# Kernel optimization log

Measured on AMD Instinct MI355X. Metric: run time of the kernel, lower is better.

The kernel has to match this reference:

```python
import jax, jax.numpy as jnp
import numpy as np

E = 4096          # num edges
M = 12            # sum(m_size) = 5+4+3
C = 64            # sphere_channels
D = 64            # m_output_channels
M0 = 5            # m_size[0]
XD = 64           # extra_m0_output_channels
EC = 128          # edge channel dims (edge_channels_list = [128,128,128])
MAIN = M * C * D          # 49152
EXTRA = M0 * C * XD       # 20480
TOTAL = MAIN + EXTRA      # 69632


def setup_inputs() -> dict:
    key = jax.random.key(0)
    ks = jax.random.split(key, 8)
    def xavier(k, shape):
        fan_in, fan_out = shape
        lim = jnp.sqrt(6.0 / (fan_in + fan_out))
        return jax.random.uniform(k, shape, jnp.float32, -lim, lim)
    return {
        "x": jax.random.normal(ks[0], (E, M, C), jnp.float32),
        "x_edge": jax.random.normal(ks[1], (E, EC), jnp.float32),
        "W1": xavier(ks[2], (EC, EC)),
        "b1": jnp.zeros((EC,), jnp.float32),
        "W2": xavier(ks[3], (EC, EC)),
        "b2": jnp.zeros((EC,), jnp.float32),
        "W3": xavier(ks[4], (EC, TOTAL)),
        "b3": jnp.zeros((TOTAL,), jnp.float32),
    }


def reference(x, x_edge, W1, b1, W2, b2, W3, b3):
    # edge MLP: Dense -> silu -> Dense -> silu -> Dense
    h = jax.nn.silu(x_edge @ W1 + b1)
    h = jax.nn.silu(h @ W2 + b2)
    edge_weights = h @ W3 + b3                      # (E, TOTAL) huge intermediate
    main_w = edge_weights[:, :MAIN].reshape(E, M, C, D)
    out = jnp.einsum('bmcd,bmc->bmd', main_w, x)    # (E, M, D)
    extra_w = edge_weights[:, MAIN:].reshape(E, M0, C, XD)
    x_0 = x[:, :M0, :]
    x_0_gating = jnp.einsum('bmcd,bmc->bd', extra_w, x_0)  # (E, XD)
    return out, x_0_gating
```

## Files before the change

### kernel.cpp

```cpp
#include <hip/hip_runtime.h>
#include <hip/hip_bf16.h>

#define E 4096
#define M 12
#define C 64
#define D 64
#define M0 5
#define XD 64
#define EC 128
#define MAIN (M*C*D)
#define EXTRA (M0*C*XD)
#define TOTAL (MAIN+EXTRA)
#define NSLICE 17
#define KDIM 8256

typedef float  f32x4  __attribute__((ext_vector_type(4)));
typedef __bf16 bf16x8 __attribute__((ext_vector_type(8)));
typedef unsigned int u32x4 __attribute__((ext_vector_type(4)));
typedef unsigned int u32x2 __attribute__((ext_vector_type(2)));

typedef const __attribute__((address_space(1))) void gvoid;
typedef __attribute__((address_space(3))) void lvoid;

__device__ __forceinline__ float silu_f(float v) { return v / (1.0f + __expf(-v)); }

__device__ __forceinline__ unsigned short f2bf(float f) {
    unsigned u = __builtin_bit_cast(unsigned, f);
    u += 0x7FFFu + ((u >> 16) & 1u);
    return (unsigned short)(u >> 16);
}
__device__ __forceinline__ unsigned pack2(float a, float b) {
    return (unsigned)f2bf(a) | ((unsigned)f2bf(b) << 16);
}
__device__ __forceinline__ float asf(unsigned u) { return __builtin_bit_cast(float, u); }

__global__ __launch_bounds__(256) void mlp_kernel(
    const float* __restrict__ x_edge, const float* __restrict__ W1,
    const float* __restrict__ b1, const float* __restrict__ W2,
    const float* __restrict__ b2, unsigned short* __restrict__ h2t)
{
    __shared__ float xe[16][128];
    __shared__ float h1s[16][128];
    const int t  = threadIdx.x;
    const int b0 = blockIdx.x * 16;
    const int j  = t & 127;
    const int rh = t >> 7;

    #pragma unroll
    for (int i = 0; i < 8; ++i) {
        int lin = t + i * 256;
        int r = lin >> 7, k = lin & 127;
        xe[r][k] = x_edge[(size_t)(b0 + r) * EC + k];
    }
    __syncthreads();
    {
        float acc[8];
        float bb = b1[j];
        #pragma unroll
        for (int it = 0; it < 8; ++it) acc[it] = bb;
        for (int k = 0; k < 128; ++k) {
            float w = W1[k * EC + j];
            #pragma unroll
            for (int it = 0; it < 8; ++it) acc[it] += xe[rh + it * 2][k] * w;
        }
        #pragma unroll
        for (int it = 0; it < 8; ++it) h1s[rh + it * 2][j] = silu_f(acc[it]);
    }
    __syncthreads();
    {
        float acc[8];
        float bb = b2[j];
        #pragma unroll
        for (int it = 0; it < 8; ++it) acc[it] = bb;
        for (int k = 0; k < 128; ++k) {
            float w = W2[k * EC + j];
            #pragma unroll
            for (int it = 0; it < 8; ++it) acc[it] += h1s[rh + it * 2][k] * w;
        }
        #pragma unroll
        for (int it = 0; it < 8; ++it)
            h2t[(size_t)j * E + (b0 + rh + it * 2)] = f2bf(silu_f(acc[it]));
    }
    if (t < 16) h2t[(size_t)128 * E + b0 + t] = 0x3F80;
}

__global__ __launch_bounds__(256) void w3t_kernel(
    const float* __restrict__ W3, const float* __restrict__ b3,
    unsigned short* __restrict__ w3t)
{
    const int k = blockIdx.x;
    const int s = blockIdx.y;
    __shared__ float tile[64][68];
    const int t = threadIdx.x;
    const float* src = ((k < 128) ? (W3 + (size_t)k * TOTAL) : b3) + s * 4096;

    const int c  = t >> 2;
    const int dp = (t & 3) * 16;
    #pragma unroll
    for (int i = 0; i < 4; ++i) {
        float4 v = *reinterpret_cast<const float4*>(src + c * 64 + dp + i * 4);
        *reinterpret_cast<float4*>(&tile[c][dp + i * 4]) = v;
    }
    __syncthreads();

    const int d  = t >> 2;
    const int cp = (t & 3) * 16;
    unsigned u[8];
    #pragma unroll
    for (int i = 0; i < 8; ++i)
        u[i] = pack2(tile[cp + 2 * i][d], tile[cp + 2 * i + 1][d]);
    unsigned short* dst = w3t + (size_t)(s * 64 + d) * KDIM + k * 64 + cp;
    *reinterpret_cast<u32x4*>(dst)     = u32x4{u[0], u[1], u[2], u[3]};
    *reinterpret_cast<u32x4*>(dst + 8) = u32x4{u[4], u[5], u[6], u[7]};
}

__global__ __launch_bounds__(256, 3) void gemm_kernel(
    const float* __restrict__ x, const unsigned short* __restrict__ h2t,
    const unsigned short* __restrict__ w3t,
    float* __restrict__ out, unsigned short* __restrict__ outp,
    float* __restrict__ gatep)
{
    __shared__ __align__(16) unsigned short h2s[65 * 256];
    __shared__ __align__(16) unsigned short Bs[2][4096];

    const int t  = threadIdx.x;
    const int w  = t >> 6;
    const int l  = t & 63;
    const int p  = l >> 4;
    const int lr = l & 15;

    const int bid  = blockIdx.x;
    const int slot = (bid & 7) * 92 + (bid >> 3);
    const int grp  = slot >> 4;
    const int bx   = slot & 15;
    int s, kz, k0, nk;
    if (grp < 36) { s = grp / 3; kz = grp % 3; k0 = kz * 43; nk = 43; }
    else { int gg = grp - 36; s = 12 + (gg >> 1); kz = gg & 1; k0 = kz * 65; nk = 65 - kz; }
    const int b0 = bx * 256;
    const int m  = (s < 12) ? s : (s - 12);

    {
        const char* h2g = (const char*)(h2t + (size_t)k0 * E + b0);
        const int total = nk * 512;
        for (int lin = t * 16; lin < total; lin += 4096) {
            int kl = lin >> 9, off = lin & 511;
            *reinterpret_cast<u32x4*>((char*)h2s + lin) =
                *reinterpret_cast<const u32x4*>(h2g + (size_t)kl * (E * 2) + off);
        }
    }

    u32x4 xa[4][2];
    #pragma unroll
    for (int rf = 0; rf < 4; ++rf)
        #pragma unroll
        for (int s2 = 0; s2 < 2; ++s2) {
            const float* xp = x + (size_t)(b0 + w * 64 + rf * 16 + lr) * (M * C)
                              + m * 64 + s2 * 32 + p * 8;
            float4 a = *reinterpret_cast<const float4*>(xp);
            float4 b = *reinterpret_cast<const float4*>(xp + 4);
            xa[rf][s2] = u32x4{pack2(a.x, a.y), pack2(a.z, a.w),
                               pack2(b.x, b.y), pack2(b.z, b.w)};
        }

    const unsigned short* gsrc[2];
    #pragma unroll
    for (int q = 0; q < 2; ++q)
        gsrc[q] = w3t + (size_t)(s * 64 + w * 16 + lr) * KDIM
                  + (size_t)k0 * 64 + (q * 4 + p) * 8;

#define STAGE(buf, kr)                                                          \
    {                                                                           \
        _Pragma("unroll")                                                       \
        for (int q = 0; q < 2; ++q)                                             \
            __builtin_amdgcn_global_load_lds(                                   \
                (gvoid*)(gsrc[q] + (size_t)(kr) * 64),                          \
                (lvoid*)(&Bs[buf][(w * 2 + q) * 512]), 16, 0, 0);               \
    }

    f32x4 acc[4][4];
    #pragma unroll
    for (int a = 0; a < 4; ++a)
        #pragma unroll
        for (int b = 0; b < 4; ++b) acc[a][b] = f32x4{0.f, 0.f, 0.f, 0.f};
    const f32x4 zf = {0.f, 0.f, 0.f, 0.f};

    STAGE(0, 0);
    __syncthreads();

    int cur = 0;
    for (int kr = 0; kr < nk; ++kr) {
        if (kr + 1 < nk) STAGE(cur ^ 1, kr + 1);

        float h[4][4];
        #pragma unroll
        for (int rf = 0; rf < 4; ++rf) {
            u32x2 hv = *reinterpret_cast<const u32x2*>(
                &h2s[kr * 256 + w * 64 + rf * 16 + p * 4]);
            h[rf][0] = asf(hv.x << 16);
            h[rf][1] = asf(hv.x & 0xFFFF0000u);
            h[rf][2] = asf(hv.y << 16);
            h[rf][3] = asf(hv.y & 0xFFFF0000u);
        }
        #pragma unroll
        for (int cf = 0; cf < 4; ++cf) {
            u32x4 B0 = *reinterpret_cast<const u32x4*>(&Bs[cur][(cf * 2 + 0) * 512 + l * 8]);
            u32x4 B1 = *reinterpret_cast<const u32x4*>(&Bs[cur][(cf * 2 + 1) * 512 + l * 8]);
            #pragma unroll
            for (int rf = 0; rf < 4; ++rf) {
                f32x4 tt = __builtin_amdgcn_mfma_f32_16x16x32_bf16(
                    __builtin_bit_cast(bf16x8, xa[rf][0]),
                    __builtin_bit_cast(bf16x8, B0), zf, 0, 0, 0);
                tt = __builtin_amdgcn_mfma_f32_16x16x32_bf16(
                    __builtin_bit_cast(bf16x8, xa[rf][1]),
                    __builtin_bit_cast(bf16x8, B1), tt, 0, 0, 0);
                acc[rf][cf][0] += h[rf][0] * tt[0];
                acc[rf][cf][1] += h[rf][1] * tt[1];
                acc[rf][cf][2] += h[rf][2] * tt[2];
                acc[rf][cf][3] += h[rf][3] * tt[3];
            }
        }
        __syncthreads();
        cur ^= 1;
    }
#undef STAGE

    if (s < 12) {
        if (kz == 0) {
            #pragma unroll
            for (int rf = 0; rf < 4; ++rf)
                #pragma unroll
                for (int cf = 0; cf < 4; ++cf)
                    #pragma unroll
                    for (int r = 0; r < 4; ++r) {
                        int b = b0 + w * 64 + rf * 16 + p * 4 + r;
                        int d = cf * 16 + lr;
                        out[(size_t)b * (M * D) + s * D + d] = acc[rf][cf][r];
                    }
        } else {
            unsigned short* ob = outp + (size_t)(kz - 1) * (E * M * D);
            #pragma unroll
            for (int rf = 0; rf < 4; ++rf)
                #pragma unroll
                for (int cf = 0; cf < 4; ++cf)
                    #pragma unroll
                    for (int r = 0; r < 4; ++r) {
                        int b = b0 + w * 64 + rf * 16 + p * 4 + r;
                        int d = cf * 16 + lr;
                        ob[(size_t)b * (M * D) + s * D + d] = f2bf(acc[rf][cf][r]);
                    }
        }
    } else {
        float* gp = gatep + (size_t)((s - 12) * 2 + kz) * (E * 64);
        #pragma unroll
        for (int rf = 0; rf < 4; ++rf)
            #pragma unroll
            for (int cf = 0; cf < 4; ++cf)
                #pragma unroll
                for (int r = 0; r < 4; ++r) {
                    int b = b0 + w * 64 + rf * 16 + p * 4 + r;
                    int d = cf * 16 + lr;
                    gp[(size_t)b * 64 + d] = acc[rf][cf][r];
                }
    }
}

__global__ __launch_bounds__(256) void reduce_kernel(
    float* __restrict__ out, const unsigned short* __restrict__ outp,
    const float* __restrict__ gatep)
{
    const int MAIN4 = E * M * D / 4;
    int i = blockIdx.x * 256 + threadIdx.x;
    if (i < MAIN4) {
        float4 a = reinterpret_cast<float4*>(out)[i];
        u32x2 p0 = *reinterpret_cast<const u32x2*>(outp + (size_t)i * 4);
        u32x2 p1 = *reinterpret_cast<const u32x2*>(outp + (size_t)E * M * D + (size_t)i * 4);
        a.x += asf(p0.x << 16)        + asf(p1.x << 16);
        a.y += asf(p0.x & 0xFFFF0000u) + asf(p1.x & 0xFFFF0000u);
        a.z += asf(p0.y << 16)        + asf(p1.y << 16);
        a.w += asf(p0.y & 0xFFFF0000u) + asf(p1.y & 0xFFFF0000u);
        reinterpret_cast<float4*>(out)[i] = a;
    } else {
        int j = i - MAIN4;
        const float4* g4 = reinterpret_cast<const float4*>(gatep);
        float4 sum = make_float4(0.f, 0.f, 0.f, 0.f);
        #pragma unroll
        for (int q = 0; q < 10; ++q) {
            float4 v = g4[(size_t)q * 65536 + j];
            sum.x += v.x; sum.y += v.y; sum.z += v.z; sum.w += v.w;
        }
        reinterpret_cast<float4*>(out + (size_t)E * M * D)[j] = sum;
    }
}

extern "C" void kernel_launch(void* const* d_in, const int* in_sizes, int n_in,
                              void* d_out, int out_size, void* d_ws, size_t ws_size,
                              hipStream_t stream)
{
    const float* x      = (const float*)d_in[0];
    const float* x_edge = (const float*)d_in[1];
    const float* W1     = (const float*)d_in[2];
    const float* b1     = (const float*)d_in[3];
    const float* W2     = (const float*)d_in[4];
    const float* b2     = (const float*)d_in[5];
    const float* W3     = (const float*)d_in[6];
    const float* b3     = (const float*)d_in[7];

    float* out = (float*)d_out;

    char* ws = (char*)d_ws;
    unsigned short* w3t   = (unsigned short*)ws;
    unsigned short* h2t   = (unsigned short*)(ws + 17965056);
    unsigned short* outp  = (unsigned short*)(ws + 19021824);
    float*          gatep = (float*)(ws + 31604736);

    mlp_kernel<<<E / 16, 256, 0, stream>>>(x_edge, W1, b1, W2, b2, h2t);
    w3t_kernel<<<dim3(129, NSLICE), 256, 0, stream>>>(W3, b3, w3t);
    gemm_kernel<<<736, 256, 0, stream>>>(x, h2t, w3t, out, outp, gatep);
    reduce_kernel<<<3328, 256, 0, stream>>>(out, outp, gatep);
}
```

Measured before the change: 140.9 us.

## Triple-buffer B tiles with explicit waitcnt pipeline and uniform 3-way K split

Replaces the double-buffered B staging with a three-stage ring and explicit vmcnt/lgkmcnt waits plus raw barriers, so global-to-LDS loads run further ahead of the MFMA loop. MFMA sections are bracketed with s_setprio. The extra-gating slices now use the same 3-way K split of 43 as the main slices, giving uniform blocks (816 instead of 736) and a smaller h2 LDS buffer. Gate partials are stored as bf16 across 15 partial buffers to cut write and reduce traffic, at some precision cost.

```diff
diff --git a/kernel.cpp b/kernel.cpp
--- a/kernel.cpp
+++ b/kernel.cpp
@@ -13,6 +13,7 @@
 #define TOTAL (MAIN+EXTRA)
 #define NSLICE 17
 #define KDIM 8256
+#define NKB 43
 
 typedef float  f32x4  __attribute__((ext_vector_type(4)));
 typedef __bf16 bf16x8 __attribute__((ext_vector_type(8)));
@@ -116,12 +117,11 @@
 
 __global__ __launch_bounds__(256, 3) void gemm_kernel(
     const float* __restrict__ x, const unsigned short* __restrict__ h2t,
-    const unsigned short* __restrict__ w3t,
-    float* __restrict__ out, unsigned short* __restrict__ outp,
-    float* __restrict__ gatep)
-{
-    __shared__ __align__(16) unsigned short h2s[65 * 256];
-    __shared__ __align__(16) unsigned short Bs[2][4096];
+    const unsigned short* __restrict__ w3t, float* __restrict__ out,
+    unsigned short* __restrict__ outp, unsigned short* __restrict__ gatep)
+{
+    __shared__ __align__(16) unsigned short h2s[NKB * 256];
+    __shared__ __align__(16) unsigned short Bs[3][4096];
 
     const int t  = threadIdx.x;
     const int w  = t >> 6;
@@ -130,19 +130,18 @@
     const int lr = l & 15;
 
     const int bid  = blockIdx.x;
-    const int slot = (bid & 7) * 92 + (bid >> 3);
+    const int slot = (bid & 7) * 102 + (bid >> 3);
     const int grp  = slot >> 4;
     const int bx   = slot & 15;
-    int s, kz, k0, nk;
-    if (grp < 36) { s = grp / 3; kz = grp % 3; k0 = kz * 43; nk = 43; }
-    else { int gg = grp - 36; s = 12 + (gg >> 1); kz = gg & 1; k0 = kz * 65; nk = 65 - kz; }
-    const int b0 = bx * 256;
-    const int m  = (s < 12) ? s : (s - 12);
+    const int s    = grp / 3;
+    const int kz   = grp % 3;
+    const int k0   = kz * NKB;
+    const int b0   = bx * 256;
+    const int m    = (s < 12) ? s : (s - 12);
 
     {
         const char* h2g = (const char*)(h2t + (size_t)k0 * E + b0);
-        const int total = nk * 512;
-        for (int lin = t * 16; lin < total; lin += 4096) {
+        for (int lin = t * 16; lin < NKB * 512; lin += 4096) {
             int kl = lin >> 9, off = lin & 511;
             *reinterpret_cast<u32x4*>((char*)h2s + lin) =
                 *reinterpret_cast<const u32x4*>(h2g + (size_t)kl * (E * 2) + off);
@@ -184,45 +183,72 @@
         for (int b = 0; b < 4; ++b) acc[a][b] = f32x4{0.f, 0.f, 0.f, 0.f};
     const f32x4 zf = {0.f, 0.f, 0.f, 0.f};
 
+#define KBODY(kr, curv)                                                         \
+    {                                                                           \
+        float h[4][4];                                                          \
+        _Pragma("unroll")                                                       \
+        for (int rf = 0; rf < 4; ++rf) {                                        \
+            u32x2 hv = *reinterpret_cast<const u32x2*>(                         \
+                &h2s[(kr) * 256 + w * 64 + rf * 16 + p * 4]);                   \
+            h[rf][0] = asf(hv.x << 16);                                         \
+            h[rf][1] = asf(hv.x & 0xFFFF0000u);                                 \
+            h[rf][2] = asf(hv.y << 16);                                         \
+            h[rf][3] = asf(hv.y & 0xFFFF0000u);                                 \
+        }                                                                       \
+        __builtin_amdgcn_s_setprio(1);                                          \
+        _Pragma("unroll")                                                       \
+        for (int cf = 0; cf < 4; ++cf) {                                        \
+            u32x4 B0 = *reinterpret_cast<const u32x4*>(                         \
+                &Bs[curv][(cf * 2 + 0) * 512 + l * 8]);                         \
+            u32x4 B1 = *reinterpret_cast<const u32x4*>(                         \
+                &Bs[curv][(cf * 2 + 1) * 512 + l * 8]);                         \
+            _Pragma("unroll")                                                   \
+            for (int rf = 0; rf < 4; ++rf) {                                    \
+                f32x4 tt = __builtin_amdgcn_mfma_f32_16x16x32_bf16(             \
+                    __builtin_bit_cast(bf16x8, xa[rf][0]),                      \
+                    __builtin_bit_cast(bf16x8, B0), zf, 0, 0, 0);               \
+                tt = __builtin_amdgcn_mfma_f32_16x16x32_bf16(                   \
+                    __builtin_bit_cast(bf16x8, xa[rf][1]),                      \
+                    __builtin_bit_cast(bf16x8, B1), tt, 0, 0, 0);               \
+                acc[rf][cf][0] += h[rf][0] * tt[0];                             \
+                acc[rf][cf][1] += h[rf][1] * tt[1];                             \
+                acc[rf][cf][2] += h[rf][2] * tt[2];                             \
+                acc[rf][cf][3] += h[rf][3] * tt[3];                             \
+            }                                                                   \
+        }                                                                       \
+        __builtin_amdgcn_s_setprio(0);                                          \
+    }
+
+    __syncthreads();
+
     STAGE(0, 0);
-    __syncthreads();
+    STAGE(1, 1);
+    STAGE(2, 2);
 
     int cur = 0;
-    for (int kr = 0; kr < nk; ++kr) {
-        if (kr + 1 < nk) STAGE(cur ^ 1, kr + 1);
-
-        float h[4][4];
-        #pragma unroll
-        for (int rf = 0; rf < 4; ++rf) {
-            u32x2 hv = *reinterpret_cast<const u32x2*>(
-                &h2s[kr * 256 + w * 64 + rf * 16 + p * 4]);
-            h[rf][0] = asf(hv.x << 16);
-            h[rf][1] = asf(hv.x & 0xFFFF0000u);
-            h[rf][2] = asf(hv.y << 16);
-            h[rf][3] = asf(hv.y & 0xFFFF0000u);
-        }
-        #pragma unroll
-        for (int cf = 0; cf < 4; ++cf) {
-            u32x4 B0 = *reinterpret_cast<const u32x4*>(&Bs[cur][(cf * 2 + 0) * 512 + l * 8]);
-            u32x4 B1 = *reinterpret_cast<const u32x4*>(&Bs[cur][(cf * 2 + 1) * 512 + l * 8]);
-            #pragma unroll
-            for (int rf = 0; rf < 4; ++rf) {
-                f32x4 tt = __builtin_amdgcn_mfma_f32_16x16x32_bf16(
-                    __builtin_bit_cast(bf16x8, xa[rf][0]),
-                    __builtin_bit_cast(bf16x8, B0), zf, 0, 0, 0);
-                tt = __builtin_amdgcn_mfma_f32_16x16x32_bf16(
-                    __builtin_bit_cast(bf16x8, xa[rf][1]),
-                    __builtin_bit_cast(bf16x8, B1), tt, 0, 0, 0);
-                acc[rf][cf][0] += h[rf][0] * tt[0];
-                acc[rf][cf][1] += h[rf][1] * tt[1];
-                acc[rf][cf][2] += h[rf][2] * tt[2];
-                acc[rf][cf][3] += h[rf][3] * tt[3];
-            }
-        }
-        __syncthreads();
-        cur ^= 1;
-    }
+    #pragma unroll 1
+    for (int kr = 0; kr < NKB - 3; ++kr) {
+        asm volatile("s_waitcnt vmcnt(4)" ::: "memory");
+        __builtin_amdgcn_s_barrier();
+        KBODY(kr, cur);
+        asm volatile("s_waitcnt lgkmcnt(0)" ::: "memory");
+        __builtin_amdgcn_s_barrier();
+        STAGE(cur, kr + 3);
+        cur = (cur == 2) ? 0 : cur + 1;
+    }
+    asm volatile("s_waitcnt vmcnt(4)" ::: "memory");
+    __builtin_amdgcn_s_barrier();
+    KBODY(NKB - 3, cur);
+    cur = (cur == 2) ? 0 : cur + 1;
+    asm volatile("s_waitcnt vmcnt(2)" ::: "memory");
+    __builtin_amdgcn_s_barrier();
+    KBODY(NKB - 2, cur);
+    cur = (cur == 2) ? 0 : cur + 1;
+    asm volatile("s_waitcnt vmcnt(0)" ::: "memory");
+    __builtin_amdgcn_s_barrier();
+    KBODY(NKB - 1, cur);
 #undef STAGE
+#undef KBODY
 
     if (s < 12) {
         if (kz == 0) {
@@ -250,7 +276,7 @@
                     }
         }
     } else {
-        float* gp = gatep + (size_t)((s - 12) * 2 + kz) * (E * 64);
+        unsigned short* gp = gatep + (size_t)((s - 12) * 3 + kz) * (E * 64);
         #pragma unroll
         for (int rf = 0; rf < 4; ++rf)
             #pragma unroll
@@ -259,14 +285,14 @@
                 for (int r = 0; r < 4; ++r) {
                     int b = b0 + w * 64 + rf * 16 + p * 4 + r;
                     int d = cf * 16 + lr;
-                    gp[(size_t)b * 64 + d] = acc[rf][cf][r];
+                    gp[(size_t)b * 64 + d] = f2bf(acc[rf][cf][r]);
                 }
     }
 }
 
 __global__ __launch_bounds__(256) void reduce_kernel(
     float* __restrict__ out, const unsigned short* __restrict__ outp,
-    const float* __restrict__ gatep)
+    const unsigned short* __restrict__ gatep)
 {
     const int MAIN4 = E * M * D / 4;
     int i = blockIdx.x * 256 + threadIdx.x;
@@ -274,19 +300,22 @@
         float4 a = reinterpret_cast<float4*>(out)[i];
         u32x2 p0 = *reinterpret_cast<const u32x2*>(outp + (size_t)i * 4);
         u32x2 p1 = *reinterpret_cast<const u32x2*>(outp + (size_t)E * M * D + (size_t)i * 4);
-        a.x += asf(p0.x << 16)        + asf(p1.x << 16);
+        a.x += asf(p0.x << 16)         + asf(p1.x << 16);
         a.y += asf(p0.x & 0xFFFF0000u) + asf(p1.x & 0xFFFF0000u);
-        a.z += asf(p0.y << 16)        + asf(p1.y << 16);
+        a.z += asf(p0.y << 16)         + asf(p1.y << 16);
         a.w += asf(p0.y & 0xFFFF0000u) + asf(p1.y & 0xFFFF0000u);
         reinterpret_cast<float4*>(out)[i] = a;
     } else {
         int j = i - MAIN4;
-        const float4* g4 = reinterpret_cast<const float4*>(gatep);
         float4 sum = make_float4(0.f, 0.f, 0.f, 0.f);
         #pragma unroll
-        for (int q = 0; q < 10; ++q) {
-            float4 v = g4[(size_t)q * 65536 + j];
-            sum.x += v.x; sum.y += v.y; sum.z += v.z; sum.w += v.w;
+        for (int q = 0; q < 15; ++q) {
+            u32x2 v = *reinterpret_cast<const u32x2*>(
+                gatep + (size_t)q * (E * 64) + (size_t)j * 4);
+            sum.x += asf(v.x << 16);
+            sum.y += asf(v.x & 0xFFFF0000u);
+            sum.z += asf(v.y << 16);
+            sum.w += asf(v.y & 0xFFFF0000u);
         }
         reinterpret_cast<float4*>(out + (size_t)E * M * D)[j] = sum;
     }
@@ -311,10 +340,10 @@
     unsigned short* w3t   = (unsigned short*)ws;
     unsigned short* h2t   = (unsigned short*)(ws + 17965056);
     unsigned short* outp  = (unsigned short*)(ws + 19021824);
-    float*          gatep = (float*)(ws + 31604736);
+    unsigned short* gatep = (unsigned short*)(ws + 31604736);
 
     mlp_kernel<<<E / 16, 256, 0, stream>>>(x_edge, W1, b1, W2, b2, h2t);
     w3t_kernel<<<dim3(129, NSLICE), 256, 0, stream>>>(W3, b3, w3t);
-    gemm_kernel<<<736, 256, 0, stream>>>(x, h2t, w3t, out, outp, gatep);
+    gemm_kernel<<<816, 256, 0, stream>>>(x, h2t, w3t, out, outp, gatep);
     reduce_kernel<<<3328, 256, 0, stream>>>(out, outp, gatep);
 }
```

Measured after the change: 146.9 us. 4.3% more time.
